# Kernel optimization log

Measured on AMD Instinct MI355X. Metric: run time of the kernel, lower is better.

The kernel has to match this reference:

```python
import jax, jax.numpy as jnp
import numpy as np

B, S, DIM, H = 8, 1024, 1024, 16
HID = 512  # FeedForward default hidden_dim=512 (module passes only dim)
DH = DIM // H
EPS = 1e-5


def setup_inputs() -> dict:
    key = jax.random.key(0)
    ks = jax.random.split(key, 12)
    s = 1.0 / np.sqrt(DIM)
    return {
        "x": jax.random.normal(ks[0], (B, S, DIM), dtype=jnp.float32),
        "Wq": jax.random.normal(ks[1], (DIM, DIM), dtype=jnp.float32) * s,
        "Wk": jax.random.normal(ks[2], (DIM, DIM), dtype=jnp.float32) * s,
        "Wv": jax.random.normal(ks[3], (DIM, DIM), dtype=jnp.float32) * s,
        "Wo": jax.random.normal(ks[4], (DIM, DIM), dtype=jnp.float32) * s,
        "ln1_g": jnp.ones((DIM,), jnp.float32),
        "ln1_b": jnp.zeros((DIM,), jnp.float32),
        "W1": jax.random.normal(ks[5], (DIM, HID), dtype=jnp.float32) * s,
        "b1": jnp.zeros((HID,), jnp.float32),
        "W2": jax.random.normal(ks[6], (HID, DIM), dtype=jnp.float32) * (1.0 / np.sqrt(HID)),
        "b2": jnp.zeros((DIM,), jnp.float32),
        "ln2_g": jnp.ones((DIM,), jnp.float32),
        "ln2_b": jnp.zeros((DIM,), jnp.float32),
    }


def _layer_norm(x, g, b):
    mu = jnp.mean(x, axis=-1, keepdims=True)
    var = jnp.mean(jnp.square(x - mu), axis=-1, keepdims=True)
    return (x - mu) * jax.lax.rsqrt(var + EPS) * g + b


def reference(x, Wq, Wk, Wv, Wo, ln1_g, ln1_b, W1, b1, W2, b2, ln2_g, ln2_b):
    # Multi-head self-attention (dropout = identity at eval)
    def heads(t):  # [B,S,DIM] -> [B,H,S,DH]
        return t.reshape(B, S, H, DH).transpose(0, 2, 1, 3)

    q = heads(x @ Wq)
    k = heads(x @ Wk)
    v = heads(x @ Wv)
    scores = jnp.einsum("bhqd,bhkd->bhqk", q, k) / jnp.sqrt(jnp.float32(DH))
    attn = jax.nn.softmax(scores, axis=-1)
    ctx = jnp.einsum("bhqk,bhkd->bhqd", attn, v)
    ctx = ctx.transpose(0, 2, 1, 3).reshape(B, S, DIM)
    mha = ctx @ Wo

    h = _layer_norm(mha + x, ln1_g, ln1_b)
    ff = jax.nn.relu(h @ W1 + b1) @ W2 + b2
    out = _layer_norm(ff + h, ln2_g, ln2_b)
    return out
```

## Files before the change

### kernel.cpp

```cpp
#include <hip/hip_runtime.h>
#include <cstdint>
#include <cstddef>

#define DEV __device__ __forceinline__

typedef __bf16 bf16x8 __attribute__((ext_vector_type(8)));
typedef __bf16 bf16x4 __attribute__((ext_vector_type(4)));
typedef short  short4v __attribute__((ext_vector_type(4)));
typedef float  f32x4  __attribute__((ext_vector_type(4)));

static constexpr int Bb  = 8;
static constexpr int S   = 1024;
static constexpr int DIM = 1024;
static constexpr int H   = 16;
static constexpr int DH  = 64;
static constexpr int HID = 512;
static constexpr int M   = Bb * S;

DEV uint16_t f2bf(float f) {
  union { float f; uint32_t u; } v; v.f = f;
  uint32_t r = v.u + 0x7fffu + ((v.u >> 16) & 1u);
  return (uint16_t)(r >> 16);
}
DEV float bf2f(uint32_t u) {
  union { uint32_t u; float f; } v; v.u = u << 16;
  return v.f;
}

DEV void gl_lds16(const uint16_t* g, uint16_t* lds) {
  __builtin_amdgcn_global_load_lds(
      (const __attribute__((address_space(1))) void*)g,
      (__attribute__((address_space(3))) void*)lds, 16, 0, 0);
}

DEV bf16x8 ld8(const uint16_t* p) { return *reinterpret_cast<const bf16x8*>(p); }

#if __has_builtin(__builtin_amdgcn_mfma_f32_16x16x16bf16_1k)
DEV f32x4 mfma16(bf16x4 a, bf16x4 b, f32x4 c) {
  return __builtin_amdgcn_mfma_f32_16x16x16bf16_1k(
      __builtin_bit_cast(short4v, a), __builtin_bit_cast(short4v, b), c, 0, 0, 0);
}
#else
DEV f32x4 mfma16(bf16x4 a, bf16x4 b, f32x4 c) {
  asm volatile("v_mfma_f32_16x16x16_bf16 %0, %1, %2, %0" : "+v"(c) : "v"(a), "v"(b));
  return c;
}
#endif

DEV int swz(int row, int col) {
  return row * 64 + (((col >> 3) ^ (row & 7)) << 3) + (col & 7);
}

__global__ __launch_bounds__(256) void prep_all(const float* __restrict__ x,
                                                uint16_t* __restrict__ x16,
                                                const float* __restrict__ Wq,
                                                const float* __restrict__ Wk,
                                                const float* __restrict__ Wv,
                                                const float* __restrict__ Wo,
                                                const float* __restrict__ W1,
                                                const float* __restrict__ W2,
                                                uint16_t* __restrict__ wqkv_t,
                                                uint16_t* __restrict__ wo_t,
                                                uint16_t* __restrict__ w1_t,
                                                uint16_t* __restrict__ w2_t) {
  int bid = blockIdx.x;
  int tid = threadIdx.x;
  if (bid < 4096) {
    int i = (bid * 256 + tid) * 8;
    const float4* p = reinterpret_cast<const float4*>(x + i);
    float4 a = p[0], b = p[1];
    uint4 pk;
    pk.x = (uint32_t)f2bf(a.x) | ((uint32_t)f2bf(a.y) << 16);
    pk.y = (uint32_t)f2bf(a.z) | ((uint32_t)f2bf(a.w) << 16);
    pk.z = (uint32_t)f2bf(b.x) | ((uint32_t)f2bf(b.y) << 16);
    pk.w = (uint32_t)f2bf(b.z) | ((uint32_t)f2bf(b.w) << 16);
    *reinterpret_cast<uint4*>(x16 + i) = pk;
    return;
  }
  bid -= 4096;
  const float* src;
  uint16_t* dst;
  int R, C, bx, by;
  if (bid < 4096) {
    int which = bid >> 10, id = bid & 1023;
    if (which == 0)      { src = Wq; dst = wqkv_t; }
    else if (which == 1) { src = Wk; dst = wqkv_t + 1048576; }
    else if (which == 2) { src = Wv; dst = wqkv_t + 2097152; }
    else                 { src = Wo; dst = wo_t; }
    R = 1024; C = 1024; bx = id & 31; by = id >> 5;
  } else if (bid < 4608) {
    int id = bid - 4096;
    src = W1; dst = w1_t; R = 1024; C = 512; bx = id & 15; by = id >> 4;
  } else {
    int id = bid - 4608;
    src = W2; dst = w2_t; R = 512; C = 1024; bx = id & 31; by = id >> 5;
  }
  __shared__ float tile[32][33];
  int c0 = bx * 32, r0 = by * 32;
  int tx = tid & 31, ty = tid >> 5;
  #pragma unroll
  for (int i = 0; i < 4; i++)
    tile[ty + i * 8][tx] = src[(size_t)(r0 + ty + i * 8) * C + c0 + tx];
  __syncthreads();
  #pragma unroll
  for (int i = 0; i < 4; i++)
    dst[(size_t)(c0 + ty + i * 8) * R + r0 + tx] = f2bf(tile[tx][ty + i * 8]);
}

template <int BIAS, int RELU, int OUT_BF16>
__global__ __launch_bounds__(256) void gemm_bt(const uint16_t* __restrict__ A,
                                               const uint16_t* __restrict__ Bt,
                                               const float* __restrict__ bias,
                                               void* __restrict__ Cout,
                                               int Mm, int N, int K) {
  __shared__ __align__(16) uint16_t As[128 * 32];
  __shared__ __align__(16) uint16_t Bs[128 * 32];
  const int tid = threadIdx.x;
  const int w = tid >> 6, l = tid & 63;
  int nwg = gridDim.x * gridDim.y;
  int lin = blockIdx.y * gridDim.x + blockIdx.x;
  if (!(nwg & 7)) lin = (lin & 7) * (nwg >> 3) + (lin >> 3);
  const int bx = lin % gridDim.x, by = lin / gridDim.x;
  const int m0 = by * 128, n0 = bx * 128;
  const int wr = (w >> 1) * 64, wc = (w & 1) * 64;
  const int wbase = w * 64;
  f32x4 acc[4][4] = {};
  const uint16_t* Ag = A + (size_t)m0 * K;
  const uint16_t* Bg = Bt + (size_t)n0 * K;

  for (int k0 = 0; k0 < K; k0 += 32) {
    __syncthreads();
    #pragma unroll
    for (int n = 0; n < 2; n++) {
      int lin2 = n * 256 + tid;
      int row = lin2 >> 2, col = (lin2 & 3) * 8;
      gl_lds16(Ag + (size_t)row * K + k0 + col, &As[(size_t)(n * 256 + wbase) * 8]);
      gl_lds16(Bg + (size_t)row * K + k0 + col, &Bs[(size_t)(n * 256 + wbase) * 8]);
    }
    __syncthreads();
    bf16x8 af[4], bfr[4];
    #pragma unroll
    for (int i = 0; i < 4; i++) {
      af[i]  = ld8(&As[(wr + i * 16 + (l & 15)) * 32 + (l >> 4) * 8]);
      bfr[i] = ld8(&Bs[(wc + i * 16 + (l & 15)) * 32 + (l >> 4) * 8]);
    }
    #pragma unroll
    for (int i = 0; i < 4; i++)
      #pragma unroll
      for (int j = 0; j < 4; j++)
        acc[i][j] = __builtin_amdgcn_mfma_f32_16x16x32_bf16(af[i], bfr[j], acc[i][j], 0, 0, 0);
  }

  const int r0 = m0 + wr + (l >> 4) * 4;
  const int c0 = n0 + wc + (l & 15);
  #pragma unroll
  for (int j = 0; j < 4; j++) {
    int col = c0 + j * 16;
    float bv = BIAS ? bias[col] : 0.0f;
    #pragma unroll
    for (int i = 0; i < 4; i++) {
      #pragma unroll
      for (int r = 0; r < 4; r++) {
        float v = acc[i][j][r] + bv;
        if (RELU) v = fmaxf(v, 0.0f);
        int row = r0 + i * 16 + r;
        if (OUT_BF16)
          ((uint16_t*)Cout)[(size_t)row * N + col] = f2bf(v);
        else
          ((float*)Cout)[(size_t)row * N + col] = v;
      }
    }
  }
}

__global__ __launch_bounds__(512, 2) void gemm256(const uint16_t* __restrict__ A,
                                                  const uint16_t* __restrict__ Bt,
                                                  uint16_t* __restrict__ Cout,
                                                  uint16_t* __restrict__ vt,
                                                  int N, int K) {
  __shared__ __align__(16) uint16_t As[2][256 * 64];
  __shared__ __align__(16) uint16_t Bs[2][256 * 64];
  const int tid = threadIdx.x;
  const int w = tid >> 6, l = tid & 63;
  const int hi = l >> 4, c = l & 15;
  int nwg = gridDim.x * gridDim.y;
  int lin = blockIdx.y * gridDim.x + blockIdx.x;
  if (!(nwg & 7)) lin = (lin & 7) * (nwg >> 3) + (lin >> 3);
  const int bx = lin % gridDim.x, by = lin / gridDim.x;
  const int m0 = by * 256, n0 = bx * 256;
  const int wr = w >> 2, wc = w & 3;
  const uint16_t* Ag = A + (size_t)m0 * K;
  const uint16_t* Bg = Bt + (size_t)n0 * K;
  f32x4 acc[8][4] = {};

  const int srow = tid >> 3, sch = tid & 7;
  auto stage = [&](int k0, int buf) {
    #pragma unroll
    for (int i = 0; i < 4; i++) {
      int row = i * 64 + srow;
      int scol = (sch ^ (row & 7)) * 8;
      gl_lds16(Ag + (size_t)row * K + k0 + scol, &As[buf][(i * 512 + w * 64) * 8]);
    }
    #pragma unroll
    for (int i = 0; i < 4; i++) {
      int row = i * 64 + srow;
      int scol = (sch ^ (row & 7)) * 8;
      gl_lds16(Bg + (size_t)row * K + k0 + scol, &Bs[buf][(i * 512 + w * 64) * 8]);
    }
  };

  stage(0, 0);
  stage(64, 1);
  asm volatile("s_waitcnt vmcnt(8)" ::: "memory");
  __builtin_amdgcn_s_barrier();

  const int NTK = K >> 6;
  for (int t = 0; t < NTK; t++) {
    const int cur = t & 1;
    const uint16_t* Ab = As[cur];
    const uint16_t* Bb = Bs[cur];
    bf16x8 bfr[4][2];
    #pragma unroll
    for (int ni = 0; ni < 4; ni++)
      #pragma unroll
      for (int kk = 0; kk < 2; kk++)
        bfr[ni][kk] = ld8(&Bb[swz(wc * 64 + ni * 16 + c, kk * 32 + hi * 8)]);
    #pragma unroll
    for (int mi = 0; mi < 8; mi++) {
      bf16x8 a0 = ld8(&Ab[swz(wr * 128 + mi * 16 + c, hi * 8)]);
      bf16x8 a1 = ld8(&Ab[swz(wr * 128 + mi * 16 + c, 32 + hi * 8)]);
      #pragma unroll
      for (int ni = 0; ni < 4; ni++) {
        acc[mi][ni] = __builtin_amdgcn_mfma_f32_16x16x32_bf16(a0, bfr[ni][0], acc[mi][ni], 0, 0, 0);
        acc[mi][ni] = __builtin_amdgcn_mfma_f32_16x16x32_bf16(a1, bfr[ni][1], acc[mi][ni], 0, 0, 0);
      }
    }
    if (t == NTK - 1) break;
    asm volatile("s_waitcnt lgkmcnt(0)" ::: "memory");
    __builtin_amdgcn_s_barrier();
    if (t + 2 < NTK) {
      stage((t + 2) << 6, cur);
      asm volatile("s_waitcnt vmcnt(8)" ::: "memory");
    } else {
      asm volatile("s_waitcnt vmcnt(0)" ::: "memory");
    }
    __builtin_amdgcn_s_barrier();
  }

  const int r0 = m0 + wr * 128 + hi * 4;
  const int c0 = n0 + wc * 64 + c;
  if (c0 >= 2048) {
    #pragma unroll
    for (int ni = 0; ni < 4; ni++) {
      int hd = c0 + ni * 16 - 2048;
      #pragma unroll
      for (int mi = 0; mi < 8; mi++) {
        int row = r0 + mi * 16;
        size_t vi = ((size_t)(row >> 10) * 1024 + hd) * 1024 + (row & 1023);
        uint2 pk;
        pk.x = (uint32_t)f2bf(acc[mi][ni][0]) | ((uint32_t)f2bf(acc[mi][ni][1]) << 16);
        pk.y = (uint32_t)f2bf(acc[mi][ni][2]) | ((uint32_t)f2bf(acc[mi][ni][3]) << 16);
        *(uint2*)&vt[vi] = pk;
      }
    }
  } else {
    #pragma unroll
    for (int mi = 0; mi < 8; mi++)
      #pragma unroll
      for (int ni = 0; ni < 4; ni++)
        #pragma unroll
        for (int r = 0; r < 4; r++)
          Cout[(size_t)(r0 + mi * 16 + r) * N + c0 + ni * 16] = f2bf(acc[mi][ni][r]);
  }
}

__global__ __launch_bounds__(256, 4) void attn9(const uint16_t* __restrict__ qkv,
                                                const uint16_t* __restrict__ vt,
                                                uint16_t* __restrict__ ctx) {
  int blk = blockIdx.x;
  int xcd = blk & 7, idx = blk >> 3;
  int qt = idx & 7;
  int bh = xcd + 8 * (idx >> 3);
  int h = bh & 15, b = bh >> 4;
  int q0 = qt * 128;
  int tid = threadIdx.x;
  int w = tid >> 6, l = tid & 63;
  int hi = l >> 4, c = l & 15;

  __shared__ __align__(16) uint16_t Klds[2][64 * 64];
  __shared__ __align__(16) uint16_t Vlds[2][64 * 64];

  const uint16_t* qbase = qkv + (size_t)(b * S + q0 + w * 32) * 3072 + h * 64;
  bf16x8 aq[2][2];
  #pragma unroll
  for (int qg = 0; qg < 2; qg++)
    #pragma unroll
    for (int dk = 0; dk < 2; dk++)
      aq[qg][dk] = ld8(qbase + (size_t)(qg * 16 + c) * 3072 + dk * 32 + hi * 8);

  f32x4 acc[2][4] = {};
  float psum[2] = {};

  const uint16_t* kgbase = qkv + (size_t)(b * S) * 3072 + 1024 + h * 64;
  const uint16_t* vgbase = vt + (size_t)(b * 16 + h) * 64 * S;

  const int lr = l >> 3, lc = l & 7;
  const int scol = (lc ^ lr) * 8;
  auto stage = [&](int kt, int buf) {
    #pragma unroll
    for (int i = 0; i < 2; i++) {
      int slab = w * 2 + i;
      gl_lds16(kgbase + (size_t)(kt + slab * 8 + lr) * 3072 + scol,
               &Klds[buf][slab * 512]);
      gl_lds16(vgbase + (size_t)(slab * 8 + lr) * S + kt + scol,
               &Vlds[buf][slab * 512]);
    }
  };

  stage(0, 0);
  asm volatile("s_waitcnt vmcnt(0)" ::: "memory");
  __syncthreads();

  constexpr float C2 = 0.125f * 1.44269504f;
  constexpr int NT = S / 64;
  for (int t = 0; t < NT; t++) {
    int cur = t & 1;
    if (t + 1 < NT) stage((t + 1) * 64, cur ^ 1);

    #pragma unroll
    for (int kb = 0; kb < 4; kb++) {
      bf16x8 kf0 = ld8(&Klds[cur][swz(kb * 16 + c, hi * 8)]);
      bf16x8 kf1 = ld8(&Klds[cur][swz(kb * 16 + c, 32 + hi * 8)]);
      bf16x4 pb[2];
      #pragma unroll
      for (int qg = 0; qg < 2; qg++) {
        f32x4 z = {0.f, 0.f, 0.f, 0.f};
        z = __builtin_amdgcn_mfma_f32_16x16x32_bf16(kf0, aq[qg][0], z, 0, 0, 0);
        z = __builtin_amdgcn_mfma_f32_16x16x32_bf16(kf1, aq[qg][1], z, 0, 0, 0);
        #pragma unroll
        for (int r = 0; r < 4; r++) {
          float p = exp2f(z[r] * C2);
          psum[qg] += p;
          pb[qg][r] = (__bf16)p;
        }
      }
      #pragma unroll
      for (int db = 0; db < 4; db++) {
        bf16x4 va = *(const bf16x4*)&Vlds[cur][swz(db * 16 + c, kb * 16 + hi * 4)];
        acc[0][db] = mfma16(va, pb[0], acc[0][db]);
        acc[1][db] = mfma16(va, pb[1], acc[1][db]);
      }
    }

    asm volatile("s_waitcnt vmcnt(0)" ::: "memory");
    __syncthreads();
  }

  #pragma unroll
  for (int qg = 0; qg < 2; qg++) {
    psum[qg] += __shfl_xor(psum[qg], 16);
    psum[qg] += __shfl_xor(psum[qg], 32);
  }

  uint16_t* Bw = &Vlds[w >> 1][(w & 1) * 2048];
  #pragma unroll
  for (int qg = 0; qg < 2; qg++) {
    float inv = 1.0f / psum[qg];
    int q = qg * 16 + c;
    #pragma unroll
    for (int db = 0; db < 4; db++) {
      uint2 pk;
      pk.x = (uint32_t)f2bf(acc[qg][db][0] * inv) |
             ((uint32_t)f2bf(acc[qg][db][1] * inv) << 16);
      pk.y = (uint32_t)f2bf(acc[qg][db][2] * inv) |
             ((uint32_t)f2bf(acc[qg][db][3] * inv) << 16);
      int chunk4 = (db * 4 + hi) ^ (q & 15);
      *(uint2*)&Bw[q * 64 + chunk4 * 4] = pk;
    }
  }
  int rrow = l >> 3, rch = l & 7;
  size_t gq0 = (size_t)(b * S + q0 + w * 32);
  #pragma unroll
  for (int it = 0; it < 4; it++) {
    int row = it * 8 + rrow;
    int k0 = (2 * rch) ^ (row & 15);
    int base = (k0 & ~1) * 4;
    uint4 v = *(const uint4*)&Bw[row * 64 + base];
    if (row & 1) { uint32_t t0 = v.x, t1 = v.y; v.x = v.z; v.y = v.w; v.z = t0; v.w = t1; }
    *(uint4*)&ctx[(gq0 + row) * DIM + h * 64 + rch * 8] = v;
  }
}

__global__ __launch_bounds__(256) void ln1_b(const uint16_t* __restrict__ a16,
                                             const uint16_t* __restrict__ x16,
                                             const float* __restrict__ g,
                                             const float* __restrict__ beta,
                                             uint16_t* __restrict__ h16) {
  int row = blockIdx.x;
  int t = threadIdx.x;
  int w = t >> 6, l = t & 63;
  uint2 av = reinterpret_cast<const uint2*>(a16 + (size_t)row * DIM)[t];
  uint2 xv = reinterpret_cast<const uint2*>(x16 + (size_t)row * DIM)[t];
  float v0 = bf2f(av.x & 0xffff) + bf2f(xv.x & 0xffff);
  float v1 = bf2f(av.x >> 16)    + bf2f(xv.x >> 16);
  float v2 = bf2f(av.y & 0xffff) + bf2f(xv.y & 0xffff);
  float v3 = bf2f(av.y >> 16)    + bf2f(xv.y >> 16);
  float s = v0 + v1 + v2 + v3;
  float sq = v0 * v0 + v1 * v1 + v2 * v2 + v3 * v3;
  #pragma unroll
  for (int off = 32; off >= 1; off >>= 1) {
    s += __shfl_xor(s, off);
    sq += __shfl_xor(sq, off);
  }
  __shared__ float ws[4], wq[4];
  if (l == 0) { ws[w] = s; wq[w] = sq; }
  __syncthreads();
  s = ws[0] + ws[1] + ws[2] + ws[3];
  sq = wq[0] + wq[1] + wq[2] + wq[3];
  float mu = s * (1.0f / DIM);
  float var = sq * (1.0f / DIM) - mu * mu;
  float rstd = rsqrtf(var + 1e-5f);
  const float4 gv = reinterpret_cast<const float4*>(g)[t];
  const float4 btv = reinterpret_cast<const float4*>(beta)[t];
  float o0 = (v0 - mu) * rstd * gv.x + btv.x;
  float o1 = (v1 - mu) * rstd * gv.y + btv.y;
  float o2 = (v2 - mu) * rstd * gv.z + btv.z;
  float o3 = (v3 - mu) * rstd * gv.w + btv.w;
  uint2 pk;
  pk.x = (uint32_t)f2bf(o0) | ((uint32_t)f2bf(o1) << 16);
  pk.y = (uint32_t)f2bf(o2) | ((uint32_t)f2bf(o3) << 16);
  reinterpret_cast<uint2*>(h16 + (size_t)row * DIM)[t] = pk;
}

__global__ __launch_bounds__(256) void ln2_b(const uint16_t* __restrict__ ff16,
                                             const uint16_t* __restrict__ h16,
                                             const float* __restrict__ g,
                                             const float* __restrict__ beta,
                                             float* __restrict__ out_f) {
  int row = blockIdx.x;
  int t = threadIdx.x;
  int w = t >> 6, l = t & 63;
  uint2 av = reinterpret_cast<const uint2*>(ff16 + (size_t)row * DIM)[t];
  uint2 hv = reinterpret_cast<const uint2*>(h16 + (size_t)row * DIM)[t];
  float v0 = bf2f(av.x & 0xffff) + bf2f(hv.x & 0xffff);
  float v1 = bf2f(av.x >> 16)    + bf2f(hv.x >> 16);
  float v2 = bf2f(av.y & 0xffff) + bf2f(hv.y & 0xffff);
  float v3 = bf2f(av.y >> 16)    + bf2f(hv.y >> 16);
  float s = v0 + v1 + v2 + v3;
  float sq = v0 * v0 + v1 * v1 + v2 * v2 + v3 * v3;
  #pragma unroll
  for (int off = 32; off >= 1; off >>= 1) {
    s += __shfl_xor(s, off);
    sq += __shfl_xor(sq, off);
  }
  __shared__ float ws[4], wq[4];
  if (l == 0) { ws[w] = s; wq[w] = sq; }
  __syncthreads();
  s = ws[0] + ws[1] + ws[2] + ws[3];
  sq = wq[0] + wq[1] + wq[2] + wq[3];
  float mu = s * (1.0f / DIM);
  float var = sq * (1.0f / DIM) - mu * mu;
  float rstd = rsqrtf(var + 1e-5f);
  const float4 gv = reinterpret_cast<const float4*>(g)[t];
  const float4 btv = reinterpret_cast<const float4*>(beta)[t];
  float4 o;
  o.x = (v0 - mu) * rstd * gv.x + btv.x;
  o.y = (v1 - mu) * rstd * gv.y + btv.y;
  o.z = (v2 - mu) * rstd * gv.z + btv.z;
  o.w = (v3 - mu) * rstd * gv.w + btv.w;
  reinterpret_cast<float4*>(out_f + (size_t)row * DIM)[t] = o;
}

extern "C" void kernel_launch(void* const* d_in, const int* in_sizes, int n_in,
                              void* d_out, int out_size, void* d_ws, size_t ws_size,
                              hipStream_t stream) {
  const float* x    = (const float*)d_in[0];
  const float* Wq   = (const float*)d_in[1];
  const float* Wk   = (const float*)d_in[2];
  const float* Wv   = (const float*)d_in[3];
  const float* Wo   = (const float*)d_in[4];
  const float* ln1g = (const float*)d_in[5];
  const float* ln1b = (const float*)d_in[6];
  const float* W1   = (const float*)d_in[7];
  const float* b1   = (const float*)d_in[8];
  const float* W2   = (const float*)d_in[9];
  const float* b2   = (const float*)d_in[10];
  const float* ln2g = (const float*)d_in[11];
  const float* ln2b = (const float*)d_in[12];
  float* out = (float*)d_out;

  char* ws = (char*)d_ws;
  uint16_t* wqkv_t = (uint16_t*)(ws + 0);
  uint16_t* wo_t   = (uint16_t*)(ws + 6291456);
  uint16_t* w1_t   = (uint16_t*)(ws + 8388608);
  uint16_t* w2_t   = (uint16_t*)(ws + 9437184);
  uint16_t* x16    = (uint16_t*)(ws + 10485760);
  uint16_t* qkv16  = (uint16_t*)(ws + 27262976);
  uint16_t* mha16  = (uint16_t*)(ws + 27262976);
  uint16_t* ff16   = (uint16_t*)(ws + 27262976);
  uint16_t* h16    = (uint16_t*)(ws + 60817408);
  uint16_t* vt16   = (uint16_t*)(ws + 77594624);
  uint16_t* mid16  = vt16;
  uint16_t* ctx16  = (uint16_t*)(ws + 94371840);

  prep_all<<<9216, 256, 0, stream>>>(x, x16, Wq, Wk, Wv, Wo, W1, W2,
                                     wqkv_t, wo_t, w1_t, w2_t);
  gemm256<<<dim3(12, 32), 512, 0, stream>>>(x16, wqkv_t, qkv16, vt16, 3072, DIM);
  attn9<<<1024, 256, 0, stream>>>(qkv16, vt16, ctx16);
  gemm_bt<0, 0, 1><<<dim3(8, 64), 256, 0, stream>>>(ctx16, wo_t, nullptr, mha16, M, DIM, DIM);
  ln1_b<<<M, 256, 0, stream>>>(mha16, x16, ln1g, ln1b, h16);
  gemm_bt<1, 1, 1><<<dim3(4, 64), 256, 0, stream>>>(h16, w1_t, b1, mid16, M, HID, DIM);
  gemm_bt<1, 0, 1><<<dim3(8, 64), 256, 0, stream>>>(mid16, w2_t, b2, ff16, M, DIM, HID);
  ln2_b<<<M, 256, 0, stream>>>(ff16, h16, ln2g, ln2b, out);
}
```

Measured before the change: 243.6 us.

## Halve QKV GEMM K-tile to 32 and move V transpose to separate kernel

The 256x256 QKV GEMM now stages K-slices of 32 instead of 64, halving LDS use per buffer, with a matching 4-chunk swizzle, likely so more workgroups can be resident or stages turn over faster. The fused V-transposed epilogue is removed; a new vtrans kernel reads V from the qkv buffer and writes the transposed layout through shared memory. This trades an extra launch and an extra read/write pass over V for a simpler, uniform GEMM epilogue, and doubles the number of barrier-synchronised K iterations.

Measured after the change: 267.7 us. 9.9% more time.

```diff
diff --git a/kernel.cpp b/kernel.cpp
--- a/kernel.cpp
+++ b/kernel.cpp
@@ -49,6 +49,9 @@
 
 DEV int swz(int row, int col) {
   return row * 64 + (((col >> 3) ^ (row & 7)) << 3) + (col & 7);
+}
+DEV int swz32(int row, int col) {
+  return row * 32 + (((col >> 3) ^ ((row >> 1) & 3)) << 3) + (col & 7);
 }
 
 __global__ __launch_bounds__(256) void prep_all(const float* __restrict__ x,
@@ -107,6 +110,28 @@
     dst[(size_t)(c0 + ty + i * 8) * R + r0 + tx] = f2bf(tile[tx][ty + i * 8]);
 }
 
+__global__ __launch_bounds__(256) void vtrans(const uint16_t* __restrict__ qkv,
+                                              uint16_t* __restrict__ vt) {
+  int bh = blockIdx.x;
+  int s0 = blockIdx.y * 64;
+  int b = bh >> 4, h = bh & 15;
+  int tid = threadIdx.x;
+  __shared__ uint16_t t[64][65];
+  #pragma unroll
+  for (int j = 0; j < 16; j++) {
+    int lin = j * 256 + tid;
+    int sl = lin >> 6, d = lin & 63;
+    t[d][sl] = qkv[(size_t)(b * S + s0 + sl) * 3072 + 2048 + h * 64 + d];
+  }
+  __syncthreads();
+  #pragma unroll
+  for (int j = 0; j < 16; j++) {
+    int lin = j * 256 + tid;
+    int dl = lin >> 6, sl = lin & 63;
+    vt[((size_t)bh * 64 + dl) * S + s0 + sl] = t[dl][sl];
+  }
+}
+
 template <int BIAS, int RELU, int OUT_BF16>
 __global__ __launch_bounds__(256) void gemm_bt(const uint16_t* __restrict__ A,
                                                const uint16_t* __restrict__ Bt,
@@ -176,10 +201,9 @@
 __global__ __launch_bounds__(512, 2) void gemm256(const uint16_t* __restrict__ A,
                                                   const uint16_t* __restrict__ Bt,
                                                   uint16_t* __restrict__ Cout,
-                                                  uint16_t* __restrict__ vt,
                                                   int N, int K) {
-  __shared__ __align__(16) uint16_t As[2][256 * 64];
-  __shared__ __align__(16) uint16_t Bs[2][256 * 64];
+  __shared__ __align__(16) uint16_t As[2][256 * 32];
+  __shared__ __align__(16) uint16_t Bs[2][256 * 32];
   const int tid = threadIdx.x;
   const int w = tid >> 6, l = tid & 63;
   const int hi = l >> 4, c = l & 15;
@@ -193,54 +217,50 @@
   const uint16_t* Bg = Bt + (size_t)n0 * K;
   f32x4 acc[8][4] = {};
 
-  const int srow = tid >> 3, sch = tid & 7;
   auto stage = [&](int k0, int buf) {
     #pragma unroll
-    for (int i = 0; i < 4; i++) {
-      int row = i * 64 + srow;
-      int scol = (sch ^ (row & 7)) * 8;
+    for (int i = 0; i < 2; i++) {
+      int slot = i * 512 + tid;
+      int row = slot >> 2, ch = slot & 3;
+      int scol = ((ch ^ ((row >> 1) & 3))) * 8;
       gl_lds16(Ag + (size_t)row * K + k0 + scol, &As[buf][(i * 512 + w * 64) * 8]);
     }
     #pragma unroll
-    for (int i = 0; i < 4; i++) {
-      int row = i * 64 + srow;
-      int scol = (sch ^ (row & 7)) * 8;
+    for (int i = 0; i < 2; i++) {
+      int slot = i * 512 + tid;
+      int row = slot >> 2, ch = slot & 3;
+      int scol = ((ch ^ ((row >> 1) & 3))) * 8;
       gl_lds16(Bg + (size_t)row * K + k0 + scol, &Bs[buf][(i * 512 + w * 64) * 8]);
     }
   };
 
   stage(0, 0);
-  stage(64, 1);
-  asm volatile("s_waitcnt vmcnt(8)" ::: "memory");
+  stage(32, 1);
+  asm volatile("s_waitcnt vmcnt(4)" ::: "memory");
   __builtin_amdgcn_s_barrier();
 
-  const int NTK = K >> 6;
+  const int NTK = K >> 5;
   for (int t = 0; t < NTK; t++) {
     const int cur = t & 1;
     const uint16_t* Ab = As[cur];
     const uint16_t* Bb = Bs[cur];
-    bf16x8 bfr[4][2];
+    bf16x8 bfr[4];
     #pragma unroll
     for (int ni = 0; ni < 4; ni++)
+      bfr[ni] = ld8(&Bb[swz32(wc * 64 + ni * 16 + c, hi * 8)]);
+    #pragma unroll
+    for (int mi = 0; mi < 8; mi++) {
+      bf16x8 a0 = ld8(&Ab[swz32(wr * 128 + mi * 16 + c, hi * 8)]);
       #pragma unroll
-      for (int kk = 0; kk < 2; kk++)
-        bfr[ni][kk] = ld8(&Bb[swz(wc * 64 + ni * 16 + c, kk * 32 + hi * 8)]);
-    #pragma unroll
-    for (int mi = 0; mi < 8; mi++) {
-      bf16x8 a0 = ld8(&Ab[swz(wr * 128 + mi * 16 + c, hi * 8)]);
-      bf16x8 a1 = ld8(&Ab[swz(wr * 128 + mi * 16 + c, 32 + hi * 8)]);
-      #pragma unroll
-      for (int ni = 0; ni < 4; ni++) {
-        acc[mi][ni] = __builtin_amdgcn_mfma_f32_16x16x32_bf16(a0, bfr[ni][0], acc[mi][ni], 0, 0, 0);
-        acc[mi][ni] = __builtin_amdgcn_mfma_f32_16x16x32_bf16(a1, bfr[ni][1], acc[mi][ni], 0, 0, 0);
-      }
+      for (int ni = 0; ni < 4; ni++)
+        acc[mi][ni] = __builtin_amdgcn_mfma_f32_16x16x32_bf16(a0, bfr[ni], acc[mi][ni], 0, 0, 0);
     }
     if (t == NTK - 1) break;
     asm volatile("s_waitcnt lgkmcnt(0)" ::: "memory");
     __builtin_amdgcn_s_barrier();
     if (t + 2 < NTK) {
-      stage((t + 2) << 6, cur);
-      asm volatile("s_waitcnt vmcnt(8)" ::: "memory");
+      stage((t + 2) << 5, cur);
+      asm volatile("s_waitcnt vmcnt(4)" ::: "memory");
     } else {
       asm volatile("s_waitcnt vmcnt(0)" ::: "memory");
     }
@@ -249,29 +269,13 @@
 
   const int r0 = m0 + wr * 128 + hi * 4;
   const int c0 = n0 + wc * 64 + c;
-  if (c0 >= 2048) {
-    #pragma unroll
-    for (int ni = 0; ni < 4; ni++) {
-      int hd = c0 + ni * 16 - 2048;
+  #pragma unroll
+  for (int mi = 0; mi < 8; mi++)
+    #pragma unroll
+    for (int ni = 0; ni < 4; ni++)
       #pragma unroll
-      for (int mi = 0; mi < 8; mi++) {
-        int row = r0 + mi * 16;
-        size_t vi = ((size_t)(row >> 10) * 1024 + hd) * 1024 + (row & 1023);
-        uint2 pk;
-        pk.x = (uint32_t)f2bf(acc[mi][ni][0]) | ((uint32_t)f2bf(acc[mi][ni][1]) << 16);
-        pk.y = (uint32_t)f2bf(acc[mi][ni][2]) | ((uint32_t)f2bf(acc[mi][ni][3]) << 16);
-        *(uint2*)&vt[vi] = pk;
-      }
-    }
-  } else {
-    #pragma unroll
-    for (int mi = 0; mi < 8; mi++)
-      #pragma unroll
-      for (int ni = 0; ni < 4; ni++)
-        #pragma unroll
-        for (int r = 0; r < 4; r++)
-          Cout[(size_t)(r0 + mi * 16 + r) * N + c0 + ni * 16] = f2bf(acc[mi][ni][r]);
-  }
+      for (int r = 0; r < 4; r++)
+        Cout[(size_t)(r0 + mi * 16 + r) * N + c0 + ni * 16] = f2bf(acc[mi][ni][r]);
 }
 
 __global__ __launch_bounds__(256, 4) void attn9(const uint16_t* __restrict__ qkv,
@@ -505,7 +509,8 @@
 
   prep_all<<<9216, 256, 0, stream>>>(x, x16, Wq, Wk, Wv, Wo, W1, W2,
                                      wqkv_t, wo_t, w1_t, w2_t);
-  gemm256<<<dim3(12, 32), 512, 0, stream>>>(x16, wqkv_t, qkv16, vt16, 3072, DIM);
+  gemm256<<<dim3(12, 32), 512, 0, stream>>>(x16, wqkv_t, qkv16, 3072, DIM);
+  vtrans<<<dim3(128, 16), 256, 0, stream>>>(qkv16, vt16);
   attn9<<<1024, 256, 0, stream>>>(qkv16, vt16, ctx16);
   gemm_bt<0, 0, 1><<<dim3(8, 64), 256, 0, stream>>>(ctx16, wo_t, nullptr, mha16, M, DIM, DIM);
   ln1_b<<<M, 256, 0, stream>>>(mha16, x16, ln1g, ln1b, h16);
```

## Unify GEMMs into a double-buffered swizzled 128x128 kernel

Applied to the files above, without the earlier changes.

Replaces the single-buffered 128x128 GEMM with a double-buffered version that uses K-step 64 and an XOR-swizzled shared-memory layout, and uses it for the output-projection and both FFN GEMMs. The 256x256 QKV GEMM is also replaced by this 128x128 kernel, giving more workgroups (1536 instead of 384) in exchange for less data reuse per tile. The aim is to overlap global loads with MFMA work and cut LDS bank conflicts in the three smaller GEMMs, but the QKV GEMM may lose efficiency from the smaller tile.

After: 221.3 us. 1.1x faster.

```diff
diff --git a/kernel.cpp b/kernel.cpp
--- a/kernel.cpp
+++ b/kernel.cpp
@@ -107,79 +107,15 @@
     dst[(size_t)(c0 + ty + i * 8) * R + r0 + tx] = f2bf(tile[tx][ty + i * 8]);
 }
 
-template <int BIAS, int RELU, int OUT_BF16>
-__global__ __launch_bounds__(256) void gemm_bt(const uint16_t* __restrict__ A,
-                                               const uint16_t* __restrict__ Bt,
-                                               const float* __restrict__ bias,
-                                               void* __restrict__ Cout,
-                                               int Mm, int N, int K) {
-  __shared__ __align__(16) uint16_t As[128 * 32];
-  __shared__ __align__(16) uint16_t Bs[128 * 32];
-  const int tid = threadIdx.x;
-  const int w = tid >> 6, l = tid & 63;
-  int nwg = gridDim.x * gridDim.y;
-  int lin = blockIdx.y * gridDim.x + blockIdx.x;
-  if (!(nwg & 7)) lin = (lin & 7) * (nwg >> 3) + (lin >> 3);
-  const int bx = lin % gridDim.x, by = lin / gridDim.x;
-  const int m0 = by * 128, n0 = bx * 128;
-  const int wr = (w >> 1) * 64, wc = (w & 1) * 64;
-  const int wbase = w * 64;
-  f32x4 acc[4][4] = {};
-  const uint16_t* Ag = A + (size_t)m0 * K;
-  const uint16_t* Bg = Bt + (size_t)n0 * K;
-
-  for (int k0 = 0; k0 < K; k0 += 32) {
-    __syncthreads();
-    #pragma unroll
-    for (int n = 0; n < 2; n++) {
-      int lin2 = n * 256 + tid;
-      int row = lin2 >> 2, col = (lin2 & 3) * 8;
-      gl_lds16(Ag + (size_t)row * K + k0 + col, &As[(size_t)(n * 256 + wbase) * 8]);
-      gl_lds16(Bg + (size_t)row * K + k0 + col, &Bs[(size_t)(n * 256 + wbase) * 8]);
-    }
-    __syncthreads();
-    bf16x8 af[4], bfr[4];
-    #pragma unroll
-    for (int i = 0; i < 4; i++) {
-      af[i]  = ld8(&As[(wr + i * 16 + (l & 15)) * 32 + (l >> 4) * 8]);
-      bfr[i] = ld8(&Bs[(wc + i * 16 + (l & 15)) * 32 + (l >> 4) * 8]);
-    }
-    #pragma unroll
-    for (int i = 0; i < 4; i++)
-      #pragma unroll
-      for (int j = 0; j < 4; j++)
-        acc[i][j] = __builtin_amdgcn_mfma_f32_16x16x32_bf16(af[i], bfr[j], acc[i][j], 0, 0, 0);
-  }
-
-  const int r0 = m0 + wr + (l >> 4) * 4;
-  const int c0 = n0 + wc + (l & 15);
-  #pragma unroll
-  for (int j = 0; j < 4; j++) {
-    int col = c0 + j * 16;
-    float bv = BIAS ? bias[col] : 0.0f;
-    #pragma unroll
-    for (int i = 0; i < 4; i++) {
-      #pragma unroll
-      for (int r = 0; r < 4; r++) {
-        float v = acc[i][j][r] + bv;
-        if (RELU) v = fmaxf(v, 0.0f);
-        int row = r0 + i * 16 + r;
-        if (OUT_BF16)
-          ((uint16_t*)Cout)[(size_t)row * N + col] = f2bf(v);
-        else
-          ((float*)Cout)[(size_t)row * N + col] = v;
-      }
-    }
-  }
-}
-
-__global__ __launch_bounds__(512, 2) void gemm256(const uint16_t* __restrict__ A,
-                                                  const uint16_t* __restrict__ Bt,
-                                                  uint16_t* __restrict__ Cout,
-                                                  uint16_t* __restrict__ vt,
-                                                  int N, int K) {
-  __shared__ __align__(16) uint16_t As[2][256 * 64];
-  __shared__ __align__(16) uint16_t Bs[2][256 * 64];
+template <int BIAS, int RELU, int FUSEV>
+__global__ __launch_bounds__(256) void gemm128p(const uint16_t* __restrict__ A,
+                                                const uint16_t* __restrict__ Bt,
+                                                const float* __restrict__ bias,
+                                                uint16_t* __restrict__ Cout,
+                                                uint16_t* __restrict__ vt,
+                                                int N, int K) {
+  __shared__ __align__(16) uint16_t As[2][128 * 64];
+  __shared__ __align__(16) uint16_t Bs[2][128 * 64];
   const int tid = threadIdx.x;
   const int w = tid >> 6, l = tid & 63;
   const int hi = l >> 4, c = l & 15;
@@ -187,26 +123,23 @@
   int lin = blockIdx.y * gridDim.x + blockIdx.x;
   if (!(nwg & 7)) lin = (lin & 7) * (nwg >> 3) + (lin >> 3);
   const int bx = lin % gridDim.x, by = lin / gridDim.x;
-  const int m0 = by * 256, n0 = bx * 256;
-  const int wr = w >> 2, wc = w & 3;
+  const int m0 = by * 128, n0 = bx * 128;
+  const int wr = (w >> 1) * 64, wc = (w & 1) * 64;
   const uint16_t* Ag = A + (size_t)m0 * K;
   const uint16_t* Bg = Bt + (size_t)n0 * K;
-  f32x4 acc[8][4] = {};
-
-  const int srow = tid >> 3, sch = tid & 7;
+  f32x4 acc[4][4] = {};
+
+  const int srow = tid >> 3;
+  const int scol = ((tid & 7) ^ (srow & 7)) * 8;
   auto stage = [&](int k0, int buf) {
     #pragma unroll
-    for (int i = 0; i < 4; i++) {
-      int row = i * 64 + srow;
-      int scol = (sch ^ (row & 7)) * 8;
-      gl_lds16(Ag + (size_t)row * K + k0 + scol, &As[buf][(i * 512 + w * 64) * 8]);
-    }
-    #pragma unroll
-    for (int i = 0; i < 4; i++) {
-      int row = i * 64 + srow;
-      int scol = (sch ^ (row & 7)) * 8;
-      gl_lds16(Bg + (size_t)row * K + k0 + scol, &Bs[buf][(i * 512 + w * 64) * 8]);
-    }
+    for (int i = 0; i < 4; i++)
+      gl_lds16(Ag + (size_t)(i * 32 + srow) * K + k0 + scol,
+               &As[buf][(i * 256 + w * 64) * 8]);
+    #pragma unroll
+    for (int i = 0; i < 4; i++)
+      gl_lds16(Bg + (size_t)(i * 32 + srow) * K + k0 + scol,
+               &Bs[buf][(i * 256 + w * 64) * 8]);
   };
 
   stage(0, 0);
@@ -219,22 +152,21 @@
     const int cur = t & 1;
     const uint16_t* Ab = As[cur];
     const uint16_t* Bb = Bs[cur];
-    bf16x8 bfr[4][2];
-    #pragma unroll
-    for (int ni = 0; ni < 4; ni++)
-      #pragma unroll
-      for (int kk = 0; kk < 2; kk++)
-        bfr[ni][kk] = ld8(&Bb[swz(wc * 64 + ni * 16 + c, kk * 32 + hi * 8)]);
-    #pragma unroll
-    for (int mi = 0; mi < 8; mi++) {
-      bf16x8 a0 = ld8(&Ab[swz(wr * 128 + mi * 16 + c, hi * 8)]);
-      bf16x8 a1 = ld8(&Ab[swz(wr * 128 + mi * 16 + c, 32 + hi * 8)]);
-      #pragma unroll
-      for (int ni = 0; ni < 4; ni++) {
-        acc[mi][ni] = __builtin_amdgcn_mfma_f32_16x16x32_bf16(a0, bfr[ni][0], acc[mi][ni], 0, 0, 0);
-        acc[mi][ni] = __builtin_amdgcn_mfma_f32_16x16x32_bf16(a1, bfr[ni][1], acc[mi][ni], 0, 0, 0);
-      }
-    }
+    bf16x8 af[4][2], bfr[4][2];
+    #pragma unroll
+    for (int i = 0; i < 4; i++)
+      #pragma unroll
+      for (int kk = 0; kk < 2; kk++) {
+        af[i][kk]  = ld8(&Ab[swz(wr + i * 16 + c, kk * 32 + hi * 8)]);
+        bfr[i][kk] = ld8(&Bb[swz(wc + i * 16 + c, kk * 32 + hi * 8)]);
+      }
+    #pragma unroll
+    for (int i = 0; i < 4; i++)
+      #pragma unroll
+      for (int j = 0; j < 4; j++) {
+        acc[i][j] = __builtin_amdgcn_mfma_f32_16x16x32_bf16(af[i][0], bfr[j][0], acc[i][j], 0, 0, 0);
+        acc[i][j] = __builtin_amdgcn_mfma_f32_16x16x32_bf16(af[i][1], bfr[j][1], acc[i][j], 0, 0, 0);
+      }
     if (t == NTK - 1) break;
     asm volatile("s_waitcnt lgkmcnt(0)" ::: "memory");
     __builtin_amdgcn_s_barrier();
@@ -247,30 +179,37 @@
     __builtin_amdgcn_s_barrier();
   }
 
-  const int r0 = m0 + wr * 128 + hi * 4;
-  const int c0 = n0 + wc * 64 + c;
-  if (c0 >= 2048) {
-    #pragma unroll
-    for (int ni = 0; ni < 4; ni++) {
-      int hd = c0 + ni * 16 - 2048;
-      #pragma unroll
-      for (int mi = 0; mi < 8; mi++) {
-        int row = r0 + mi * 16;
+  const int r0 = m0 + wr + hi * 4;
+  const int c0 = n0 + wc + c;
+  if (FUSEV && c0 >= 2048) {
+    #pragma unroll
+    for (int j = 0; j < 4; j++) {
+      int hd = c0 + j * 16 - 2048;
+      #pragma unroll
+      for (int i = 0; i < 4; i++) {
+        int row = r0 + i * 16;
         size_t vi = ((size_t)(row >> 10) * 1024 + hd) * 1024 + (row & 1023);
         uint2 pk;
-        pk.x = (uint32_t)f2bf(acc[mi][ni][0]) | ((uint32_t)f2bf(acc[mi][ni][1]) << 16);
-        pk.y = (uint32_t)f2bf(acc[mi][ni][2]) | ((uint32_t)f2bf(acc[mi][ni][3]) << 16);
+        pk.x = (uint32_t)f2bf(acc[i][j][0]) | ((uint32_t)f2bf(acc[i][j][1]) << 16);
+        pk.y = (uint32_t)f2bf(acc[i][j][2]) | ((uint32_t)f2bf(acc[i][j][3]) << 16);
         *(uint2*)&vt[vi] = pk;
       }
     }
   } else {
     #pragma unroll
-    for (int mi = 0; mi < 8; mi++)
-      #pragma unroll
-      for (int ni = 0; ni < 4; ni++)
+    for (int j = 0; j < 4; j++) {
+      int col = c0 + j * 16;
+      float bv = BIAS ? bias[col] : 0.0f;
+      #pragma unroll
+      for (int i = 0; i < 4; i++) {
         #pragma unroll
-        for (int r = 0; r < 4; r++)
-          Cout[(size_t)(r0 + mi * 16 + r) * N + c0 + ni * 16] = f2bf(acc[mi][ni][r]);
+        for (int r = 0; r < 4; r++) {
+          float v = acc[i][j][r] + bv;
+          if (RELU) v = fmaxf(v, 0.0f);
+          Cout[(size_t)(r0 + i * 16 + r) * N + col] = f2bf(v);
+        }
+      }
+    }
   }
 }
 
@@ -505,11 +444,15 @@
 
   prep_all<<<9216, 256, 0, stream>>>(x, x16, Wq, Wk, Wv, Wo, W1, W2,
                                      wqkv_t, wo_t, w1_t, w2_t);
-  gemm256<<<dim3(12, 32), 512, 0, stream>>>(x16, wqkv_t, qkv16, vt16, 3072, DIM);
+  gemm128p<0, 0, 1><<<dim3(24, 64), 256, 0, stream>>>(x16, wqkv_t, nullptr,
+                                                      qkv16, vt16, 3072, DIM);
   attn9<<<1024, 256, 0, stream>>>(qkv16, vt16, ctx16);
-  gemm_bt<0, 0, 1><<<dim3(8, 64), 256, 0, stream>>>(ctx16, wo_t, nullptr, mha16, M, DIM, DIM);
+  gemm128p<0, 0, 0><<<dim3(8, 64), 256, 0, stream>>>(ctx16, wo_t, nullptr,
+                                                     mha16, nullptr, DIM, DIM);
   ln1_b<<<M, 256, 0, stream>>>(mha16, x16, ln1g, ln1b, h16);
-  gemm_bt<1, 1, 1><<<dim3(4, 64), 256, 0, stream>>>(h16, w1_t, b1, mid16, M, HID, DIM);
-  gemm_bt<1, 0, 1><<<dim3(8, 64), 256, 0, stream>>>(mid16, w2_t, b2, ff16, M, DIM, HID);
+  gemm128p<1, 1, 0><<<dim3(4, 64), 256, 0, stream>>>(h16, w1_t, b1,
+                                                     mid16, nullptr, HID, DIM);
+  gemm128p<1, 0, 0><<<dim3(8, 64), 256, 0, stream>>>(mid16, w2_t, b2,
+                                                     ff16, nullptr, DIM, HID);
   ln2_b<<<M, 256, 0, stream>>>(ff16, h16, ln2g, ln2b, out);
 }
```
